# Kernel optimization log

Measured on AMD Instinct MI355X. Metric: run time of the kernel, lower is better.

The kernel has to match this reference:

```python
import jax, jax.numpy as jnp
import numpy as np

H, C = 4, 32          # heads, per-head channels (hidden_dim = 128)
HID = H * C
NC, NM, E, DIN = 100000, 20000, 400000, 64


def _gat_conv(x_src, x_dst, src, dst, Wsrc, Wdst, asrc, adst, bias):
    """PyG-style bipartite GATConv: gather -> leaky-relu attention -> segment softmax -> scatter."""
    n_dst = x_dst.shape[0]
    hs = (x_src @ Wsrc).reshape(-1, H, C)            # [Ns, H, C]
    hd = (x_dst @ Wdst).reshape(-1, H, C)            # [Nd, H, C]
    a_s = jnp.sum(hs * asrc, axis=-1)                # [Ns, H]
    a_d = jnp.sum(hd * adst, axis=-1)                # [Nd, H]
    e = jax.nn.leaky_relu(a_s[src] + a_d[dst], 0.2)  # [E, H]
    m = jax.ops.segment_max(e, dst, num_segments=n_dst)
    m = jnp.where(jnp.isfinite(m), m, 0.0)           # isolated dst nodes -> -inf max
    ex = jnp.exp(e - m[dst])
    den = jax.ops.segment_sum(ex, dst, num_segments=n_dst)
    alpha = ex / (den[dst] + 1e-16)                  # per-destination segment softmax
    out = jax.ops.segment_sum(hs[src] * alpha[:, :, None], dst, num_segments=n_dst)
    return out.reshape(n_dst, HID) + bias            # concat heads + bias


def _mlp2(x, W1, b1, W2, b2):
    return jax.nn.relu(x @ W1 + b1) @ W2 + b2


def setup_inputs():
    key = jax.random.key(0)
    ks = iter(jax.random.split(key, 80))
    def rn(shape, s):
        return jax.random.normal(next(ks), shape, dtype=jnp.float32) * s
    inp = {}
    inp['x_card'] = rn((NC, DIN), 1.0)
    inp['x_merchant'] = rn((NM, DIN), 1.0)
    for l, din in ((0, DIN), (1, HID)):
        for et in ('cm', 'mc'):
            p = 'l%d_%s_' % (l, et)
            g = (2.0 / (din + HID)) ** 0.5
            inp[p + 'Wsrc'] = rn((din, HID), g)
            inp[p + 'Wdst'] = rn((din, HID), g)
            inp[p + 'asrc'] = rn((H, C), 0.1)
            inp[p + 'adst'] = rn((H, C), 0.1)
            inp[p + 'b'] = jnp.zeros((HID,), jnp.float32)
    for nt in ('card', 'merchant'):
        inp['attw_' + nt] = rn((HID, 1), 0.05)
        inp['attb_' + nt] = jnp.zeros((1,), jnp.float32)
    for nt in ('card', 'mer'):
        inp['cls_%s_W1' % nt] = rn((HID, HID // 2), 0.05)
        inp['cls_%s_b1' % nt] = jnp.zeros((HID // 2,), jnp.float32)
        inp['cls_%s_W2' % nt] = rn((HID // 2, 2), 0.05)
        inp['cls_%s_b2' % nt] = jnp.zeros((2,), jnp.float32)
    inp['risk_W1'] = rn((HID, HID // 2), 0.05)
    inp['risk_b1'] = jnp.zeros((HID // 2,), jnp.float32)
    inp['risk_W2'] = rn((HID // 2, 1), 0.05)
    inp['risk_b2'] = jnp.zeros((1,), jnp.float32)
    inp['cm_src'] = jax.random.randint(next(ks), (E,), 0, NC, dtype=jnp.int32)
    inp['cm_dst'] = jax.random.randint(next(ks), (E,), 0, NM, dtype=jnp.int32)
    inp['mc_src'] = jax.random.randint(next(ks), (E,), 0, NM, dtype=jnp.int32)
    inp['mc_dst'] = jax.random.randint(next(ks), (E,), 0, NC, dtype=jnp.int32)
    return inp


def reference(x_card, x_merchant,
              l0_cm_Wsrc, l0_cm_Wdst, l0_cm_asrc, l0_cm_adst, l0_cm_b,
              l0_mc_Wsrc, l0_mc_Wdst, l0_mc_asrc, l0_mc_adst, l0_mc_b,
              l1_cm_Wsrc, l1_cm_Wdst, l1_cm_asrc, l1_cm_adst, l1_cm_b,
              l1_mc_Wsrc, l1_mc_Wdst, l1_mc_asrc, l1_mc_adst, l1_mc_b,
              attw_card, attb_card, attw_merchant, attb_merchant,
              cls_card_W1, cls_card_b1, cls_card_W2, cls_card_b2,
              cls_mer_W1, cls_mer_b1, cls_mer_W2, cls_mer_b2,
              risk_W1, risk_b1, risk_W2, risk_b2,
              cm_src, cm_dst, mc_src, mc_dst):
    xc, xm = x_card, x_merchant
    # HeteroConv layer 0 (each dst type receives exactly one edge type, so mean-aggr is identity)
    xm1 = _gat_conv(xc, xm, cm_src, cm_dst, l0_cm_Wsrc, l0_cm_Wdst, l0_cm_asrc, l0_cm_adst, l0_cm_b)
    xc1 = _gat_conv(xm, xc, mc_src, mc_dst, l0_mc_Wsrc, l0_mc_Wdst, l0_mc_asrc, l0_mc_adst, l0_mc_b)
    # HeteroConv layer 1
    xm2 = _gat_conv(xc1, xm1, cm_src, cm_dst, l1_cm_Wsrc, l1_cm_Wdst, l1_cm_asrc, l1_cm_adst, l1_cm_b)
    xc2 = _gat_conv(xm1, xc1, mc_src, mc_dst, l1_mc_Wsrc, l1_mc_Wdst, l1_mc_asrc, l1_mc_adst, l1_mc_b)
    # graph-level attention: softmax over the node dimension (dim=0), then reweight
    xc2 = xc2 * jax.nn.softmax(xc2 @ attw_card + attb_card, axis=0)
    xm2 = xm2 * jax.nn.softmax(xm2 @ attw_merchant + attb_merchant, axis=0)
    pred_c = _mlp2(xc2, cls_card_W1, cls_card_b1, cls_card_W2, cls_card_b2)
    pred_m = _mlp2(xm2, cls_mer_W1, cls_mer_b1, cls_mer_W2, cls_mer_b2)
    risk_c = jax.nn.sigmoid(_mlp2(xc2, risk_W1, risk_b1, risk_W2, risk_b2))[:, 0]
    risk_m = jax.nn.sigmoid(_mlp2(xm2, risk_W1, risk_b1, risk_W2, risk_b2))[:, 0]
    return (xc2, xm2, pred_c, pred_m, risk_c, risk_m)
```

## Files before the change

### kernel.cpp

```cpp
#include <hip/hip_runtime.h>

typedef _Float16 f16;
typedef _Float16 f16x2 __attribute__((ext_vector_type(2)));
typedef _Float16 f16x4 __attribute__((ext_vector_type(4)));
typedef _Float16 f16x8 __attribute__((ext_vector_type(8)));
typedef float floatx4 __attribute__((ext_vector_type(4)));

constexpr int NC = 100000;
constexpr int NM = 20000;
constexpr int NE = 400000;

constexpr int OFF_XM2 = NC * 128;
constexpr int OFF_PC  = OFF_XM2 + NM * 128;
constexpr int OFF_PM  = OFF_PC + NC * 2;
constexpr int OFF_RC  = OFF_PM + NM * 2;
constexpr int OFF_RM  = OFF_RC + NC;

__device__ __forceinline__ int bpermi(int v, int srclane) {
  return __builtin_amdgcn_ds_bpermute(srclane << 2, v);
}
__device__ __forceinline__ float bpermf(float v, int srclane) {
  int r = __builtin_amdgcn_ds_bpermute(srclane << 2, __builtin_bit_cast(int, v));
  return __builtin_bit_cast(float, r);
}

__global__ void __launch_bounds__(256) k_prep(
    int* zero_base, int nzero, int* stats_i,
    const float* W0, const float* a0, float* v0,
    const float* W1, const float* a1, float* v1,
    const float* W2, const float* a2, float* v2,
    const float* W3, const float* a3, float* v3,
    const float* cb1, const float* mb1, const float* rb1, float* bC, float* bM,
    const float* S0, const float* S1, const float* S2, const float* S3,
    const float* c1, const float* m1, const float* r1,
    f16* BfL0cm, f16* BfL0mc, f16* BfL1cm, f16* BfL1mc, f16* BfC, f16* BfM) {
  int b = blockIdx.x, t = threadIdx.x;
  if (b < 256) {
    for (int i = b * 256 + t; i < nzero + 4; i += 256 * 256) {
      if (i < nzero) zero_base[i] = 0; else stats_i[i - nzero] = 0;
    }
  } else if (b == 256) {
    const float* Wd[4] = {W0, W1, W2, W3};
    const float* ad[4] = {a0, a1, a2, a3};
    float* vd[4] = {v0, v1, v2, v3};
    for (int idx = t; idx < 1536; idx += 256) {
      int mat, base;
      if (idx < 256)       { mat = 0; base = 0; }
      else if (idx < 512)  { mat = 1; base = 256; }
      else if (idx < 1024) { mat = 2; base = 512; }
      else                 { mat = 3; base = 1024; }
      int local = idx - base, k = local >> 2, h = local & 3;
      const float* W = Wd[mat]; const float* a = ad[mat];
      float s = 0.f;
      for (int c = 0; c < 32; ++c) s += W[k * 128 + h * 32 + c] * a[h * 32 + c];
      vd[mat][local] = s;
    }
    if (t < 128) {
      bC[t] = (t < 64) ? cb1[t] : rb1[t - 64];
      bM[t] = (t < 64) ? mb1[t] : rb1[t - 64];
    }
  } else {
    int s = b - 257;
    const float* Wp = nullptr; const float* cA = nullptr; const float* cB = nullptr;
    f16* dst; int kt;
    if (s < 2)       { Wp = S0; dst = BfL0cm; kt = s; }
    else if (s < 4)  { Wp = S1; dst = BfL0mc; kt = s - 2; }
    else if (s < 8)  { Wp = S2; dst = BfL1cm; kt = s - 4; }
    else if (s < 12) { Wp = S3; dst = BfL1mc; kt = s - 8; }
    else if (s < 16) { cA = c1; cB = r1; dst = BfC; kt = s - 12; }
    else             { cA = m1; cB = r1; dst = BfM; kt = s - 16; }
    for (int e = t; e < 512; e += 256) {
      int lane = e & 63, ct = e >> 6;
      int m = lane & 15, q = lane >> 4;
      int col = ct * 16 + m;
      f16x8 frag;
      #pragma unroll
      for (int j = 0; j < 8; ++j) {
        int k = kt * 32 + q * 8 + j;
        float val = Wp ? Wp[k * 128 + col]
                       : (col < 64 ? cA[k * 64 + col] : cB[k * 64 + (col - 64)]);
        frag[j] = (f16)val;
      }
      *reinterpret_cast<f16x8*>(&dst[(size_t)((kt * 8 + ct) * 64 + lane) * 8]) = frag;
    }
  }
}

__global__ void k_hist(const int* cm_dst, const int* mc_dst, int* cnt_cm, int* cnt_mc) {
  int i = blockIdx.x * blockDim.x + threadIdx.x;
  int stride = gridDim.x * blockDim.x;
  for (; i < NE; i += stride) {
    atomicAdd(&cnt_cm[cm_dst[i]], 1);
    atomicAdd(&cnt_mc[mc_dst[i]], 1);
  }
}

__global__ void __launch_bounds__(256) k_scan1(const int* cnt_cm, const int* cnt_mc,
                                               int* offs_cm, int* offs_mc, int* parts) {
  int b = blockIdx.x;
  const int* cnt; int* offs; int n, chunk;
  if (b < 20) { cnt = cnt_cm; offs = offs_cm; n = NM; chunk = b; }
  else        { cnt = cnt_mc; offs = offs_mc; n = NC; chunk = b - 20; }
  int t = threadIdx.x;
  int base = chunk * 1024;
  int v[4]; int tsum = 0;
  #pragma unroll
  for (int j = 0; j < 4; ++j) {
    int idx = base + t * 4 + j;
    v[j] = (idx < n) ? cnt[idx] : 0;
    tsum += v[j];
  }
  __shared__ int sd[256];
  sd[t] = tsum; __syncthreads();
  for (int off = 1; off < 256; off <<= 1) {
    int x = (t >= off) ? sd[t - off] : 0;
    __syncthreads();
    sd[t] += x;
    __syncthreads();
  }
  int excl = sd[t] - tsum;
  int r = excl;
  #pragma unroll
  for (int j = 0; j < 4; ++j) {
    int idx = base + t * 4 + j;
    if (idx < n) offs[idx] = r;
    r += v[j];
  }
  if (t == 0) parts[b] = sd[255];
}

__global__ void __launch_bounds__(256) k_scan2(int* parts) {
  int b = blockIdx.x;
  int base = (b == 0) ? 0 : 20;
  int n = (b == 0) ? 20 : 98;
  int t = threadIdx.x;
  __shared__ int sd[128];
  int v = 0;
  if (t < 128) { v = (t < n) ? parts[base + t] : 0; sd[t] = v; }
  __syncthreads();
  for (int off = 1; off < 128; off <<= 1) {
    int x = 0;
    if (t < 128 && t >= off) x = sd[t - off];
    __syncthreads();
    if (t < 128) sd[t] += x;
    __syncthreads();
  }
  if (t < 128 && t < n) parts[base + t] = sd[t] - v;
}

__global__ void k_scan3(int* offs_cm, int* offs_mc, int* cur_cm, int* cur_mc, const int* parts) {
  int i = blockIdx.x * blockDim.x + threadIdx.x;
  if (i < NM) {
    int val = offs_cm[i] + parts[i >> 10];
    offs_cm[i] = val; cur_cm[i] = val;
  } else if (i < NM + NC) {
    int j = i - NM;
    int val = offs_mc[j] + parts[20 + (j >> 10)];
    offs_mc[j] = val; cur_mc[j] = val;
  }
  if (i == 0) { offs_cm[NM] = NE; offs_mc[NC] = NE; }
}

__global__ void k_scatter(const int* cm_src, const int* cm_dst,
                          const int* mc_src, const int* mc_dst,
                          int* cur_cm, int* cur_mc, int* csr_cm, int* csr_mc) {
  int i = blockIdx.x * blockDim.x + threadIdx.x;
  int stride = gridDim.x * blockDim.x;
  for (; i < NE; i += stride) {
    int p = atomicAdd(&cur_cm[cm_dst[i]], 1);
    csr_cm[p] = cm_src[i];
    int q = atomicAdd(&cur_mc[mc_dst[i]], 1);
    csr_mc[q] = mc_src[i];
  }
}

struct GemmSide {
  const float* x; const f16* Bf;
  const float* asrc; const float* v; f16* hs; float* asO; float* adO;
  const float* bias; const float* wnum; const float* den; float* outx;
  const float* W2; const float* B2; const float* w2r; const float* b2r;
  float* pred; float* risk;
  int M;
};

template<int K, int EPI>
__global__ void __launch_bounds__(256) k_gemm(GemmSide A, GemmSide B, int gridA) {
  constexpr int PP = K + 8;
  constexpr int F4 = K / 4;
  __shared__ f16 xs16[64 * PP];
  const bool isA = (int)blockIdx.x < gridA;
  GemmSide S = isA ? A : B;
  const int blk = isA ? (int)blockIdx.x : (int)blockIdx.x - gridA;
  const int rows0 = blk * 64;
  const int t = (int)threadIdx.x;
  float invden_s = 0.f;
  if constexpr (EPI == 1) invden_s = 1.0f / S.den[0];
  const float4* x4 = reinterpret_cast<const float4*>(S.x);
  #pragma unroll
  for (int ii = 0; ii < (64 * F4) / 256; ++ii) {
    int idx = t + ii * 256;
    int r = idx / F4, f = idx % F4;
    int gr = rows0 + r;
    float4 val = {0.f, 0.f, 0.f, 0.f};
    if (gr < S.M) val = x4[(size_t)gr * F4 + f];
    f16x4 hv; hv.x = (f16)val.x; hv.y = (f16)val.y; hv.z = (f16)val.z; hv.w = (f16)val.w;
    *reinterpret_cast<f16x4*>(&xs16[r * PP + f * 4]) = hv;
    if constexpr (EPI == 1) {
      if (gr < S.M) {
        float w = S.wnum[gr] * invden_s;
        float4 ov = {val.x * w, val.y * w, val.z * w, val.w * w};
        *reinterpret_cast<float4*>(&S.outx[(size_t)gr * 128 + f * 4]) = ov;
      }
    }
  }
  __syncthreads();
  const int lane = t & 63, w = t >> 6;
  const int m = lane & 15, q = lane >> 4;
  const int rbase = w * 16;
  floatx4 acc[8];
  #pragma unroll
  for (int ct = 0; ct < 8; ++ct) acc[ct] = {0.f, 0.f, 0.f, 0.f};
  const f16x8* Bf8 = reinterpret_cast<const f16x8*>(S.Bf);
  #pragma unroll
  for (int kt = 0; kt < K / 32; ++kt) {
    f16x8 a = *reinterpret_cast<const f16x8*>(&xs16[(rbase + m) * PP + kt * 32 + q * 8]);
    #pragma unroll
    for (int ct = 0; ct < 8; ++ct) {
      f16x8 b = Bf8[(kt * 8 + ct) * 64 + lane];
      acc[ct] = __builtin_amdgcn_mfma_f32_16x16x32_f16(a, b, acc[ct], 0, 0, 0);
    }
  }
  if constexpr (EPI == 0) {
    #pragma unroll
    for (int reg = 0; reg < 4; ++reg) {
      int gr = rows0 + rbase + q * 4 + reg;
      bool ok = gr < S.M;
      #pragma unroll
      for (int cp = 0; cp < 4; ++cp) {
        float v0 = acc[2 * cp][reg], v1 = acc[2 * cp + 1][reg];
        float w0 = __shfl_xor(v0, 1), w1 = __shfl_xor(v1, 1);
        bool even = (m & 1) == 0;
        f16x2 pr;
        pr.x = (f16)(even ? v0 : w1);
        pr.y = (f16)(even ? w0 : v1);
        int col = even ? (2 * cp) * 16 + m : (2 * cp + 1) * 16 + m - 1;
        if (ok) *reinterpret_cast<f16x2*>(&S.hs[(size_t)gr * 128 + col]) = pr;
      }
    }
    float as0[4], as1[4];
    #pragma unroll
    for (int h = 0; h < 4; ++h) { as0[h] = S.asrc[h * 32 + m]; as1[h] = S.asrc[h * 32 + 16 + m]; }
    #pragma unroll
    for (int reg = 0; reg < 4; ++reg) {
      float p[4];
      #pragma unroll
      for (int h = 0; h < 4; ++h)
        p[h] = acc[2 * h][reg] * as0[h] + acc[2 * h + 1][reg] * as1[h];
      #pragma unroll
      for (int off = 1; off < 16; off <<= 1) {
        #pragma unroll
        for (int h = 0; h < 4; ++h) p[h] += __shfl_xor(p[h], off);
      }
      int gr = rows0 + rbase + q * 4 + reg;
      if (m == 0 && gr < S.M) {
        float4 pv = {p[0], p[1], p[2], p[3]};
        *reinterpret_cast<float4*>(&S.asO[gr * 4]) = pv;
      }
    }
    float qd[4] = {0.f, 0.f, 0.f, 0.f};
    const float4* v4p = reinterpret_cast<const float4*>(S.v);
    constexpr int KS = K / 4;
    #pragma unroll
    for (int i = 0; i < KS; ++i) {
      int k = q * KS + i;
      float xv = (float)xs16[(rbase + m) * PP + k];
      float4 vk = v4p[k];
      qd[0] += xv * vk.x; qd[1] += xv * vk.y; qd[2] += xv * vk.z; qd[3] += xv * vk.w;
    }
    #pragma unroll
    for (int h = 0; h < 4; ++h) {
      qd[h] += __shfl_xor(qd[h], 16);
      qd[h] += __shfl_xor(qd[h], 32);
    }
    int gr2 = rows0 + rbase + m;
    if (q == 0 && gr2 < S.M) {
      float4 qv = {qd[0], qd[1], qd[2], qd[3]};
      *reinterpret_cast<float4*>(&S.adO[gr2 * 4]) = qv;
    }
  } else {
    float wn[4];
    #pragma unroll
    for (int reg = 0; reg < 4; ++reg) {
      int gr = rows0 + rbase + q * 4 + reg;
      wn[reg] = (gr < S.M) ? S.wnum[gr] * invden_s : 0.f;
    }
    float bct[8], w2c0[4], w2c1[4], w2rv[4];
    #pragma unroll
    for (int ct = 0; ct < 8; ++ct) bct[ct] = S.bias[ct * 16 + m];
    #pragma unroll
    for (int ct = 0; ct < 4; ++ct) {
      int col = ct * 16 + m;
      w2c0[ct] = S.W2[col * 2];
      w2c1[ct] = S.W2[col * 2 + 1];
      w2rv[ct] = S.w2r[col];
    }
    #pragma unroll
    for (int reg = 0; reg < 4; ++reg) {
      float p0 = 0.f, p1 = 0.f, rr = 0.f;
      #pragma unroll
      for (int ct = 0; ct < 4; ++ct) {
        float hv = fmaxf(acc[ct][reg] * wn[reg] + bct[ct], 0.f);
        p0 += hv * w2c0[ct];
        p1 += hv * w2c1[ct];
      }
      #pragma unroll
      for (int ct = 4; ct < 8; ++ct) {
        float hv = fmaxf(acc[ct][reg] * wn[reg] + bct[ct], 0.f);
        rr += hv * w2rv[ct - 4];
      }
      #pragma unroll
      for (int off = 1; off < 16; off <<= 1) {
        p0 += __shfl_xor(p0, off);
        p1 += __shfl_xor(p1, off);
        rr += __shfl_xor(rr, off);
      }
      int gr = rows0 + rbase + q * 4 + reg;
      if (m == 0 && gr < S.M) {
        float2 pp = {p0 + S.B2[0], p1 + S.B2[1]};
        *reinterpret_cast<float2*>(&S.pred[gr * 2]) = pp;
        float z = rr + S.b2r[0];
        S.risk[gr] = 1.f / (1.f + __expf(-z));
      }
    }
  }
}

struct AggSide {
  const int* offs; const int* csr; const float* as_; const float* ad;
  const f16* hs; const float* bias; float* out;
  const float* attw; const float* attb; float* logv;
};

__global__ void __launch_bounds__(256) k_agg(AggSide A, AggSide B, int ndstA, int ntot) {
  const int wid = (int)blockIdx.x * 4 + ((int)threadIdx.x >> 6);
  if (wid >= ntot) return;
  const bool isA = wid < ndstA;
  const AggSide S = isA ? A : B;
  const int d = isA ? wid : wid - ndstA;
  const int lane = (int)threadIdx.x & 63;
  const int we = lane >> 2, wh = lane & 3;
  const int ep = lane >> 5;
  const int c4 = lane & 31;
  const int gh = c4 >> 3;
  const int c8 = c4 << 3;
  const int wh4 = wh << 2;
  const int beg = __builtin_amdgcn_readfirstlane(S.offs[d]);
  const int end = __builtin_amdgcn_readfirstlane(S.offs[d + 1]);
  const float adv = S.ad[d * 4 + wh];
  const char* __restrict__ hsb = (const char*)S.hs;
  const char* __restrict__ asb = (const char*)S.as_;
  float m_run = -1e30f, den = 0.f;
  float acc0 = 0.f, acc1 = 0.f, acc2 = 0.f, acc3 = 0.f;
  for (int base = beg; base < end; base += 16) {
    const int n = min(16, end - base);
    int sb = 0; float e = -1e30f;
    if (we < n) {
      int s = S.csr[base + we];
      sb = s << 8;
      float asv = *reinterpret_cast<const float*>(asb + (unsigned)((s << 4) + wh4));
      float ev = asv + adv;
      e = (ev > 0.f) ? ev : 0.2f * ev;
    }
    float cm = e;
    cm = fmaxf(cm, __shfl_xor(cm, 4));
    cm = fmaxf(cm, __shfl_xor(cm, 8));
    if (n > 4) cm = fmaxf(cm, __shfl_xor(cm, 16));
    if (n > 8) cm = fmaxf(cm, __shfl_xor(cm, 32));
    const float m_new = fmaxf(m_run, cm);
    const float scale = __expf(m_run - m_new);
    const float w = __expf(e - m_new);
    float ws = w;
    ws += __shfl_xor(ws, 4);
    ws += __shfl_xor(ws, 8);
    if (n > 4) ws += __shfl_xor(ws, 16);
    if (n > 8) ws += __shfl_xor(ws, 32);
    den = den * scale + ws;
    m_run = m_new;
    const float sg = bpermf(scale, gh);
    acc0 *= sg; acc1 *= sg; acc2 *= sg; acc3 *= sg;
    int j = 0;
    for (; j + 8 <= n; j += 8) {
      int i0 = (j + ep) << 2, i1 = (j + 2 + ep) << 2;
      int i2 = (j + 4 + ep) << 2, i3 = (j + 6 + ep) << 2;
      int s0 = bpermi(sb, i0);
      int s1 = bpermi(sb, i1);
      int s2 = bpermi(sb, i2);
      int s3 = bpermi(sb, i3);
      f16x4 h0 = *reinterpret_cast<const f16x4*>(hsb + (unsigned)(s0 + c8));
      f16x4 h1 = *reinterpret_cast<const f16x4*>(hsb + (unsigned)(s1 + c8));
      f16x4 h2 = *reinterpret_cast<const f16x4*>(hsb + (unsigned)(s2 + c8));
      f16x4 h3 = *reinterpret_cast<const f16x4*>(hsb + (unsigned)(s3 + c8));
      float w0 = bpermf(w, i0 + gh);
      float w1 = bpermf(w, i1 + gh);
      float w2 = bpermf(w, i2 + gh);
      float w3 = bpermf(w, i3 + gh);
      acc0 += w0 * (float)h0.x; acc1 += w0 * (float)h0.y;
      acc2 += w0 * (float)h0.z; acc3 += w0 * (float)h0.w;
      acc0 += w1 * (float)h1.x; acc1 += w1 * (float)h1.y;
      acc2 += w1 * (float)h1.z; acc3 += w1 * (float)h1.w;
      acc0 += w2 * (float)h2.x; acc1 += w2 * (float)h2.y;
      acc2 += w2 * (float)h2.z; acc3 += w2 * (float)h2.w;
      acc0 += w3 * (float)h3.x; acc1 += w3 * (float)h3.y;
      acc2 += w3 * (float)h3.z; acc3 += w3 * (float)h3.w;
    }
    for (; j + 4 <= n; j += 4) {
      int i0 = (j + ep) << 2, i1 = (j + 2 + ep) << 2;
      int s0 = bpermi(sb, i0);
      int s1 = bpermi(sb, i1);
      f16x4 h0 = *reinterpret_cast<const f16x4*>(hsb + (unsigned)(s0 + c8));
      f16x4 h1 = *reinterpret_cast<const f16x4*>(hsb + (unsigned)(s1 + c8));
      float w0 = bpermf(w, i0 + gh);
      float w1 = bpermf(w, i1 + gh);
      acc0 += w0 * (float)h0.x; acc1 += w0 * (float)h0.y;
      acc2 += w0 * (float)h0.z; acc3 += w0 * (float)h0.w;
      acc0 += w1 * (float)h1.x; acc1 += w1 * (float)h1.y;
      acc2 += w1 * (float)h1.z; acc3 += w1 * (float)h1.w;
    }
    for (; j < n; j += 2) {
      int i0 = (j + ep) << 2;
      int s0 = bpermi(sb, i0);
      f16x4 h0 = *reinterpret_cast<const f16x4*>(hsb + (unsigned)(s0 + c8));
      float w0 = bpermf(w, i0 + gh);
      acc0 += w0 * (float)h0.x; acc1 += w0 * (float)h0.y;
      acc2 += w0 * (float)h0.z; acc3 += w0 * (float)h0.w;
    }
  }
  acc0 += __shfl_xor(acc0, 32);
  acc1 += __shfl_xor(acc1, 32);
  acc2 += __shfl_xor(acc2, 32);
  acc3 += __shfl_xor(acc3, 32);
  const float deng = bpermf(den, gh);
  const float invden = (deng > 0.f) ? 1.f / deng : 0.f;
  const float4 b4 = *reinterpret_cast<const float4*>(&S.bias[c4 * 4]);
  float o0 = acc0 * invden + b4.x;
  float o1 = acc1 * invden + b4.y;
  float o2 = acc2 * invden + b4.z;
  float o3 = acc3 * invden + b4.w;
  if (ep == 0) {
    float4 o = {o0, o1, o2, o3};
    *reinterpret_cast<float4*>(&S.out[d * 128 + c4 * 4]) = o;
  }
  if (S.attw) {
    const float4 aw = *reinterpret_cast<const float4*>(&S.attw[c4 * 4]);
    float sl = o0 * aw.x + o1 * aw.y + o2 * aw.z + o3 * aw.w;
    sl += __shfl_xor(sl, 1);
    sl += __shfl_xor(sl, 2);
    sl += __shfl_xor(sl, 4);
    sl += __shfl_xor(sl, 8);
    sl += __shfl_xor(sl, 16);
    if (lane == 0) S.logv[d] = sl + S.attb[0];
  }
}

__global__ void __launch_bounds__(1024) k_stats(const float* logc, const float* logm, float* stats) {
  const float* src = (blockIdx.x == 0) ? logc : logm;
  int n = (blockIdx.x == 0) ? NC : NM;
  float m = -1e30f;
  for (int i = threadIdx.x; i < n; i += 1024) m = fmaxf(m, src[i]);
  __shared__ float sd[1024];
  sd[threadIdx.x] = m; __syncthreads();
  for (int off = 512; off > 0; off >>= 1) {
    if ((int)threadIdx.x < off) sd[threadIdx.x] = fmaxf(sd[threadIdx.x], sd[threadIdx.x + off]);
    __syncthreads();
  }
  if (threadIdx.x == 0) stats[blockIdx.x] = sd[0];
}

__global__ void __launch_bounds__(256) k_expsum(float* logc, float* logm, float* stats) {
  bool card = (int)blockIdx.x < 256;
  float* logv = card ? logc : logm;
  int n = card ? NC : NM;
  float mx = card ? stats[0] : stats[1];
  int b0 = card ? (int)blockIdx.x : (int)blockIdx.x - 256;
  int nb = card ? 256 : 64;
  float local = 0.f;
  for (int i = b0 * 256 + (int)threadIdx.x; i < n; i += nb * 256) {
    float e = __expf(logv[i] - mx);
    logv[i] = e;
    local += e;
  }
  __shared__ float sd[256];
  sd[threadIdx.x] = local; __syncthreads();
  for (int off = 128; off > 0; off >>= 1) {
    if ((int)threadIdx.x < off) sd[threadIdx.x] += sd[threadIdx.x + off];
    __syncthreads();
  }
  if (threadIdx.x == 0) atomicAdd(card ? &stats[2] : &stats[3], sd[0]);
}

extern "C" void kernel_launch(void* const* d_in, const int* in_sizes, int n_in,
                              void* d_out, int out_size, void* d_ws, size_t ws_size,
                              hipStream_t stream) {
  (void)in_sizes; (void)n_in; (void)out_size; (void)ws_size;
  const float* x_card    = (const float*)d_in[0];
  const float* x_mer     = (const float*)d_in[1];
  const float* l0cm_Wsrc = (const float*)d_in[2];
  const float* l0cm_Wdst = (const float*)d_in[3];
  const float* l0cm_asrc = (const float*)d_in[4];
  const float* l0cm_adst = (const float*)d_in[5];
  const float* l0cm_b    = (const float*)d_in[6];
  const float* l0mc_Wsrc = (const float*)d_in[7];
  const float* l0mc_Wdst = (const float*)d_in[8];
  const float* l0mc_asrc = (const float*)d_in[9];
  const float* l0mc_adst = (const float*)d_in[10];
  const float* l0mc_b    = (const float*)d_in[11];
  const float* l1cm_Wsrc = (const float*)d_in[12];
  const float* l1cm_Wdst = (const float*)d_in[13];
  const float* l1cm_asrc = (const float*)d_in[14];
  const float* l1cm_adst = (const float*)d_in[15];
  const float* l1cm_b    = (const float*)d_in[16];
  const float* l1mc_Wsrc = (const float*)d_in[17];
  const float* l1mc_Wdst = (const float*)d_in[18];
  const float* l1mc_asrc = (const float*)d_in[19];
  const float* l1mc_adst = (const float*)d_in[20];
  const float* l1mc_b    = (const float*)d_in[21];
  const float* attw_c    = (const float*)d_in[22];
  const float* attb_c    = (const float*)d_in[23];
  const float* attw_m    = (const float*)d_in[24];
  const float* attb_m    = (const float*)d_in[25];
  const float* clsc_W1   = (const float*)d_in[26];
  const float* clsc_b1   = (const float*)d_in[27];
  const float* clsc_W2   = (const float*)d_in[28];
  const float* clsc_b2   = (const float*)d_in[29];
  const float* clsm_W1   = (const float*)d_in[30];
  const float* clsm_b1   = (const float*)d_in[31];
  const float* clsm_W2   = (const float*)d_in[32];
  const float* clsm_b2   = (const float*)d_in[33];
  const float* risk_W1   = (const float*)d_in[34];
  const float* risk_b1   = (const float*)d_in[35];
  const float* risk_W2   = (const float*)d_in[36];
  const float* risk_b2   = (const float*)d_in[37];
  const int*   cm_src    = (const int*)d_in[38];
  const int*   cm_dst    = (const int*)d_in[39];
  const int*   mc_src    = (const int*)d_in[40];
  const int*   mc_dst    = (const int*)d_in[41];
  float* out = (float*)d_out;

  float* base = (float*)d_ws;
  size_t o = 0;
  auto alloc = [&](size_t n) { float* p = base + o; o += (n + 3) & ~size_t(3); return p; };
  float* hs_card = alloc((size_t)NC * 128);
  float* xc1     = alloc((size_t)NC * 128);
  float* hs_mer  = alloc((size_t)NM * 128);
  float* xm1     = alloc((size_t)NM * 128);
  float* as_card = alloc((size_t)NC * 4);
  float* ad_card = alloc((size_t)NC * 4);
  float* as_mer  = alloc((size_t)NM * 4);
  float* ad_mer  = alloc((size_t)NM * 4);
  float* v_l0cm  = alloc(512);
  float* v_l0mc  = alloc(512);
  float* v_l1cm  = alloc(512);
  float* v_l1mc  = alloc(512);
  float* bC      = alloc(128);
  float* bM      = alloc(128);
  f16* Bf_l0cm = (f16*)alloc(64 * 128 / 2);
  f16* Bf_l0mc = (f16*)alloc(64 * 128 / 2);
  f16* Bf_l1cm = (f16*)alloc(128 * 128 / 2);
  f16* Bf_l1mc = (f16*)alloc(128 * 128 / 2);
  f16* Bf_catC = (f16*)alloc(128 * 128 / 2);
  f16* Bf_catM = (f16*)alloc(128 * 128 / 2);
  float* logc    = alloc(NC);
  float* logm    = alloc(NM);
  float* stats   = alloc(4);
  int* cnt_cm  = (int*)alloc(NM);
  int* cnt_mc  = (int*)alloc(NC);
  int* offs_cm = (int*)alloc(NM + 1);
  int* offs_mc = (int*)alloc(NC + 1);
  int* cur_cm  = (int*)alloc(NM);
  int* cur_mc  = (int*)alloc(NC);
  int* parts   = (int*)alloc(128);
  int* csr_cm  = (int*)alloc(NE);
  int* csr_mc  = (int*)alloc(NE);

  const dim3 B256(256);
  k_prep<<<dim3(277), B256, 0, stream>>>(
      cnt_cm, NM + NC, (int*)stats,
      l0cm_Wdst, l0cm_adst, v_l0cm, l0mc_Wdst, l0mc_adst, v_l0mc,
      l1cm_Wdst, l1cm_adst, v_l1cm, l1mc_Wdst, l1mc_adst, v_l1mc,
      clsc_b1, clsm_b1, risk_b1, bC, bM,
      l0cm_Wsrc, l0mc_Wsrc, l1cm_Wsrc, l1mc_Wsrc,
      clsc_W1, clsm_W1, risk_W1,
      Bf_l0cm, Bf_l0mc, Bf_l1cm, Bf_l1mc, Bf_catC, Bf_catM);
  k_hist<<<dim3(512), B256, 0, stream>>>(cm_dst, mc_dst, cnt_cm, cnt_mc);
  k_scan1<<<dim3(118), B256, 0, stream>>>(cnt_cm, cnt_mc, offs_cm, offs_mc, parts);
  k_scan2<<<dim3(2), B256, 0, stream>>>(parts);
  k_scan3<<<dim3(469), B256, 0, stream>>>(offs_cm, offs_mc, cur_cm, cur_mc, parts);
  k_scatter<<<dim3(512), B256, 0, stream>>>(cm_src, cm_dst, mc_src, mc_dst,
                                            cur_cm, cur_mc, csr_cm, csr_mc);
  const int gA = (NC + 63) / 64;
  const int gB = (NM + 63) / 64;
  const int NTOT = NM + NC;
  const int gAgg = (NTOT + 3) / 4;

  GemmSide sA, sB;
  AggSide aA, aB;
  sA = {x_card, Bf_l0cm, l0cm_asrc, v_l0mc, (f16*)hs_card, as_card, ad_card,
        nullptr, nullptr, nullptr, nullptr, nullptr, nullptr, nullptr, nullptr,
        nullptr, nullptr, NC};
  sB = {x_mer, Bf_l0mc, l0mc_asrc, v_l0cm, (f16*)hs_mer, as_mer, ad_mer,
        nullptr, nullptr, nullptr, nullptr, nullptr, nullptr, nullptr, nullptr,
        nullptr, nullptr, NM};
  k_gemm<64, 0><<<dim3(gA + gB), B256, 0, stream>>>(sA, sB, gA);
  aA = {offs_cm, csr_cm, as_card, ad_mer, (const f16*)hs_card, l0cm_b, xm1,
        nullptr, nullptr, nullptr};
  aB = {offs_mc, csr_mc, as_mer, ad_card, (const f16*)hs_mer, l0mc_b, xc1,
        nullptr, nullptr, nullptr};
  k_agg<<<dim3(gAgg), B256, 0, stream>>>(aA, aB, NM, NTOT);
  sA = {xc1, Bf_l1cm, l1cm_asrc, v_l1mc, (f16*)hs_card, as_card, ad_card,
        nullptr, nullptr, nullptr, nullptr, nullptr, nullptr, nullptr, nullptr,
        nullptr, nullptr, NC};
  sB = {xm1, Bf_l1mc, l1mc_asrc, v_l1cm, (f16*)hs_mer, as_mer, ad_mer,
        nullptr, nullptr, nullptr, nullptr, nullptr, nullptr, nullptr, nullptr,
        nullptr, nullptr, NM};
  k_gemm<128, 0><<<dim3(gA + gB), B256, 0, stream>>>(sA, sB, gA);
  aA = {offs_cm, csr_cm, as_card, ad_mer, (const f16*)hs_card, l1cm_b, xm1,
        attw_m, attb_m, logm};
  aB = {offs_mc, csr_mc, as_mer, ad_card, (const f16*)hs_mer, l1mc_b, xc1,
        attw_c, attb_c, logc};
  k_agg<<<dim3(gAgg), B256, 0, stream>>>(aA, aB, NM, NTOT);
  k_stats<<<dim3(2), dim3(1024), 0, stream>>>(logc, logm, stats);
  k_expsum<<<dim3(320), B256, 0, stream>>>(logc, logm, stats);
  sA = {xc1, Bf_catC, nullptr, nullptr, nullptr, nullptr, nullptr,
        bC, logc, stats + 2, out,
        clsc_W2, clsc_b2, risk_W2, risk_b2,
        out + OFF_PC, out + OFF_RC, NC};
  sB = {xm1, Bf_catM, nullptr, nullptr, nullptr, nullptr, nullptr,
        bM, logm, stats + 3, out + OFF_XM2,
        clsm_W2, clsm_b2, risk_W2, risk_b2,
        out + OFF_PM, out + OFF_RM, NM};
  k_gemm<128, 1><<<dim3(gA + gB), B256, 0, stream>>>(sA, sB, gA);
}
```

Before: 509.7 us.

## Pack two card destinations per wave in GAT aggregation kernel

```diff
diff --git a/kernel.cpp b/kernel.cpp
--- a/kernel.cpp
+++ b/kernel.cpp
@@ -341,124 +341,228 @@
   const float* attw; const float* attb; float* logv;
 };
 
-__global__ void __launch_bounds__(256) k_agg(AggSide A, AggSide B, int ndstA, int ntot) {
+__global__ void __launch_bounds__(256) k_agg(AggSide A, AggSide B,
+                                             int ndstA, int ndstB, int nwaves) {
   const int wid = (int)blockIdx.x * 4 + ((int)threadIdx.x >> 6);
-  if (wid >= ntot) return;
-  const bool isA = wid < ndstA;
-  const AggSide S = isA ? A : B;
-  const int d = isA ? wid : wid - ndstA;
+  if (wid >= nwaves) return;
   const int lane = (int)threadIdx.x & 63;
-  const int we = lane >> 2, wh = lane & 3;
-  const int ep = lane >> 5;
-  const int c4 = lane & 31;
-  const int gh = c4 >> 3;
-  const int c8 = c4 << 3;
-  const int wh4 = wh << 2;
-  const int beg = __builtin_amdgcn_readfirstlane(S.offs[d]);
-  const int end = __builtin_amdgcn_readfirstlane(S.offs[d + 1]);
-  const float adv = S.ad[d * 4 + wh];
-  const char* __restrict__ hsb = (const char*)S.hs;
-  const char* __restrict__ asb = (const char*)S.as_;
-  float m_run = -1e30f, den = 0.f;
-  float acc0 = 0.f, acc1 = 0.f, acc2 = 0.f, acc3 = 0.f;
-  for (int base = beg; base < end; base += 16) {
-    const int n = min(16, end - base);
-    int sb = 0; float e = -1e30f;
-    if (we < n) {
-      int s = S.csr[base + we];
-      sb = s << 8;
-      float asv = *reinterpret_cast<const float*>(asb + (unsigned)((s << 4) + wh4));
-      float ev = asv + adv;
-      e = (ev > 0.f) ? ev : 0.2f * ev;
-    }
-    float cm = e;
-    cm = fmaxf(cm, __shfl_xor(cm, 4));
-    cm = fmaxf(cm, __shfl_xor(cm, 8));
-    if (n > 4) cm = fmaxf(cm, __shfl_xor(cm, 16));
-    if (n > 8) cm = fmaxf(cm, __shfl_xor(cm, 32));
-    const float m_new = fmaxf(m_run, cm);
-    const float scale = __expf(m_run - m_new);
-    const float w = __expf(e - m_new);
-    float ws = w;
-    ws += __shfl_xor(ws, 4);
-    ws += __shfl_xor(ws, 8);
-    if (n > 4) ws += __shfl_xor(ws, 16);
-    if (n > 8) ws += __shfl_xor(ws, 32);
-    den = den * scale + ws;
-    m_run = m_new;
-    const float sg = bpermf(scale, gh);
-    acc0 *= sg; acc1 *= sg; acc2 *= sg; acc3 *= sg;
-    int j = 0;
-    for (; j + 8 <= n; j += 8) {
-      int i0 = (j + ep) << 2, i1 = (j + 2 + ep) << 2;
-      int i2 = (j + 4 + ep) << 2, i3 = (j + 6 + ep) << 2;
-      int s0 = bpermi(sb, i0);
-      int s1 = bpermi(sb, i1);
-      int s2 = bpermi(sb, i2);
-      int s3 = bpermi(sb, i3);
-      f16x4 h0 = *reinterpret_cast<const f16x4*>(hsb + (unsigned)(s0 + c8));
-      f16x4 h1 = *reinterpret_cast<const f16x4*>(hsb + (unsigned)(s1 + c8));
-      f16x4 h2 = *reinterpret_cast<const f16x4*>(hsb + (unsigned)(s2 + c8));
-      f16x4 h3 = *reinterpret_cast<const f16x4*>(hsb + (unsigned)(s3 + c8));
-      float w0 = bpermf(w, i0 + gh);
-      float w1 = bpermf(w, i1 + gh);
-      float w2 = bpermf(w, i2 + gh);
-      float w3 = bpermf(w, i3 + gh);
-      acc0 += w0 * (float)h0.x; acc1 += w0 * (float)h0.y;
-      acc2 += w0 * (float)h0.z; acc3 += w0 * (float)h0.w;
-      acc0 += w1 * (float)h1.x; acc1 += w1 * (float)h1.y;
-      acc2 += w1 * (float)h1.z; acc3 += w1 * (float)h1.w;
-      acc0 += w2 * (float)h2.x; acc1 += w2 * (float)h2.y;
-      acc2 += w2 * (float)h2.z; acc3 += w2 * (float)h2.w;
-      acc0 += w3 * (float)h3.x; acc1 += w3 * (float)h3.y;
-      acc2 += w3 * (float)h3.z; acc3 += w3 * (float)h3.w;
-    }
-    for (; j + 4 <= n; j += 4) {
-      int i0 = (j + ep) << 2, i1 = (j + 2 + ep) << 2;
-      int s0 = bpermi(sb, i0);
-      int s1 = bpermi(sb, i1);
-      f16x4 h0 = *reinterpret_cast<const f16x4*>(hsb + (unsigned)(s0 + c8));
-      f16x4 h1 = *reinterpret_cast<const f16x4*>(hsb + (unsigned)(s1 + c8));
-      float w0 = bpermf(w, i0 + gh);
-      float w1 = bpermf(w, i1 + gh);
-      acc0 += w0 * (float)h0.x; acc1 += w0 * (float)h0.y;
-      acc2 += w0 * (float)h0.z; acc3 += w0 * (float)h0.w;
-      acc0 += w1 * (float)h1.x; acc1 += w1 * (float)h1.y;
-      acc2 += w1 * (float)h1.z; acc3 += w1 * (float)h1.w;
-    }
-    for (; j < n; j += 2) {
-      int i0 = (j + ep) << 2;
-      int s0 = bpermi(sb, i0);
-      f16x4 h0 = *reinterpret_cast<const f16x4*>(hsb + (unsigned)(s0 + c8));
-      float w0 = bpermf(w, i0 + gh);
-      acc0 += w0 * (float)h0.x; acc1 += w0 * (float)h0.y;
-      acc2 += w0 * (float)h0.z; acc3 += w0 * (float)h0.w;
-    }
-  }
-  acc0 += __shfl_xor(acc0, 32);
-  acc1 += __shfl_xor(acc1, 32);
-  acc2 += __shfl_xor(acc2, 32);
-  acc3 += __shfl_xor(acc3, 32);
-  const float deng = bpermf(den, gh);
-  const float invden = (deng > 0.f) ? 1.f / deng : 0.f;
-  const float4 b4 = *reinterpret_cast<const float4*>(&S.bias[c4 * 4]);
-  float o0 = acc0 * invden + b4.x;
-  float o1 = acc1 * invden + b4.y;
-  float o2 = acc2 * invden + b4.z;
-  float o3 = acc3 * invden + b4.w;
-  if (ep == 0) {
-    float4 o = {o0, o1, o2, o3};
-    *reinterpret_cast<float4*>(&S.out[d * 128 + c4 * 4]) = o;
-  }
-  if (S.attw) {
-    const float4 aw = *reinterpret_cast<const float4*>(&S.attw[c4 * 4]);
-    float sl = o0 * aw.x + o1 * aw.y + o2 * aw.z + o3 * aw.w;
-    sl += __shfl_xor(sl, 1);
-    sl += __shfl_xor(sl, 2);
-    sl += __shfl_xor(sl, 4);
-    sl += __shfl_xor(sl, 8);
-    sl += __shfl_xor(sl, 16);
-    if (lane == 0) S.logv[d] = sl + S.attb[0];
+  if (wid < ndstA) {
+    const AggSide S = A;
+    const int d = wid;
+    const int we = lane >> 2, wh = lane & 3;
+    const int ep = lane >> 5;
+    const int c4 = lane & 31;
+    const int gh = c4 >> 3;
+    const int c8 = c4 << 3;
+    const int wh4 = wh << 2;
+    const int beg = __builtin_amdgcn_readfirstlane(S.offs[d]);
+    const int end = __builtin_amdgcn_readfirstlane(S.offs[d + 1]);
+    const float adv = S.ad[d * 4 + wh];
+    const char* __restrict__ hsb = (const char*)S.hs;
+    const char* __restrict__ asb = (const char*)S.as_;
+    float m_run = -1e30f, den = 0.f;
+    float acc0 = 0.f, acc1 = 0.f, acc2 = 0.f, acc3 = 0.f;
+    for (int base = beg; base < end; base += 16) {
+      const int n = min(16, end - base);
+      int sb = 0; float e = -1e30f;
+      if (we < n) {
+        int s = S.csr[base + we];
+        sb = s << 8;
+        float asv = *reinterpret_cast<const float*>(asb + (unsigned)((s << 4) + wh4));
+        float ev = asv + adv;
+        e = (ev > 0.f) ? ev : 0.2f * ev;
+      }
+      float cm = e;
+      cm = fmaxf(cm, __shfl_xor(cm, 4));
+      cm = fmaxf(cm, __shfl_xor(cm, 8));
+      if (n > 4) cm = fmaxf(cm, __shfl_xor(cm, 16));
+      if (n > 8) cm = fmaxf(cm, __shfl_xor(cm, 32));
+      const float m_new = fmaxf(m_run, cm);
+      const float scale = __expf(m_run - m_new);
+      const float w = __expf(e - m_new);
+      float ws = w;
+      ws += __shfl_xor(ws, 4);
+      ws += __shfl_xor(ws, 8);
+      if (n > 4) ws += __shfl_xor(ws, 16);
+      if (n > 8) ws += __shfl_xor(ws, 32);
+      den = den * scale + ws;
+      m_run = m_new;
+      const float sg = bpermf(scale, gh);
+      acc0 *= sg; acc1 *= sg; acc2 *= sg; acc3 *= sg;
+      int j = 0;
+      for (; j + 8 <= n; j += 8) {
+        int i0 = (j + ep) << 2, i1 = (j + 2 + ep) << 2;
+        int i2 = (j + 4 + ep) << 2, i3 = (j + 6 + ep) << 2;
+        int s0 = bpermi(sb, i0);
+        int s1 = bpermi(sb, i1);
+        int s2 = bpermi(sb, i2);
+        int s3 = bpermi(sb, i3);
+        f16x4 h0 = *reinterpret_cast<const f16x4*>(hsb + (unsigned)(s0 + c8));
+        f16x4 h1 = *reinterpret_cast<const f16x4*>(hsb + (unsigned)(s1 + c8));
+        f16x4 h2 = *reinterpret_cast<const f16x4*>(hsb + (unsigned)(s2 + c8));
+        f16x4 h3 = *reinterpret_cast<const f16x4*>(hsb + (unsigned)(s3 + c8));
+        float w0 = bpermf(w, i0 + gh);
+        float w1 = bpermf(w, i1 + gh);
+        float w2 = bpermf(w, i2 + gh);
+        float w3 = bpermf(w, i3 + gh);
+        acc0 += w0 * (float)h0.x; acc1 += w0 * (float)h0.y;
+        acc2 += w0 * (float)h0.z; acc3 += w0 * (float)h0.w;
+        acc0 += w1 * (float)h1.x; acc1 += w1 * (float)h1.y;
+        acc2 += w1 * (float)h1.z; acc3 += w1 * (float)h1.w;
+        acc0 += w2 * (float)h2.x; acc1 += w2 * (float)h2.y;
+        acc2 += w2 * (float)h2.z; acc3 += w2 * (float)h2.w;
+        acc0 += w3 * (float)h3.x; acc1 += w3 * (float)h3.y;
+        acc2 += w3 * (float)h3.z; acc3 += w3 * (float)h3.w;
+      }
+      for (; j + 4 <= n; j += 4) {
+        int i0 = (j + ep) << 2, i1 = (j + 2 + ep) << 2;
+        int s0 = bpermi(sb, i0);
+        int s1 = bpermi(sb, i1);
+        f16x4 h0 = *reinterpret_cast<const f16x4*>(hsb + (unsigned)(s0 + c8));
+        f16x4 h1 = *reinterpret_cast<const f16x4*>(hsb + (unsigned)(s1 + c8));
+        float w0 = bpermf(w, i0 + gh);
+        float w1 = bpermf(w, i1 + gh);
+        acc0 += w0 * (float)h0.x; acc1 += w0 * (float)h0.y;
+        acc2 += w0 * (float)h0.z; acc3 += w0 * (float)h0.w;
+        acc0 += w1 * (float)h1.x; acc1 += w1 * (float)h1.y;
+        acc2 += w1 * (float)h1.z; acc3 += w1 * (float)h1.w;
+      }
+      for (; j < n; j += 2) {
+        int i0 = (j + ep) << 2;
+        int s0 = bpermi(sb, i0);
+        f16x4 h0 = *reinterpret_cast<const f16x4*>(hsb + (unsigned)(s0 + c8));
+        float w0 = bpermf(w, i0 + gh);
+        acc0 += w0 * (float)h0.x; acc1 += w0 * (float)h0.y;
+        acc2 += w0 * (float)h0.z; acc3 += w0 * (float)h0.w;
+      }
+    }
+    acc0 += __shfl_xor(acc0, 32);
+    acc1 += __shfl_xor(acc1, 32);
+    acc2 += __shfl_xor(acc2, 32);
+    acc3 += __shfl_xor(acc3, 32);
+    const float deng = bpermf(den, gh);
+    const float invden = (deng > 0.f) ? 1.f / deng : 0.f;
+    const float4 b4 = *reinterpret_cast<const float4*>(&S.bias[c4 * 4]);
+    float o0 = acc0 * invden + b4.x;
+    float o1 = acc1 * invden + b4.y;
+    float o2 = acc2 * invden + b4.z;
+    float o3 = acc3 * invden + b4.w;
+    if (ep == 0) {
+      float4 o = {o0, o1, o2, o3};
+      *reinterpret_cast<float4*>(&S.out[d * 128 + c4 * 4]) = o;
+    }
+    if (S.attw) {
+      const float4 aw = *reinterpret_cast<const float4*>(&S.attw[c4 * 4]);
+      float sl = o0 * aw.x + o1 * aw.y + o2 * aw.z + o3 * aw.w;
+      sl += __shfl_xor(sl, 1);
+      sl += __shfl_xor(sl, 2);
+      sl += __shfl_xor(sl, 4);
+      sl += __shfl_xor(sl, 8);
+      sl += __shfl_xor(sl, 16);
+      if (lane == 0) S.logv[d] = sl + S.attb[0];
+    }
+  } else {
+    const AggSide S = B;
+    const int p = wid - ndstA;
+    const int half32 = lane & 32;
+    const int l5 = lane & 31;
+    int d = p * 2 + (lane >> 5);
+    const bool dok = d < ndstB;
+    if (!dok) d = ndstB - 1;
+    const int we = l5 >> 2, wh = l5 & 3;
+    const int gh = l5 >> 3;
+    const int c8 = l5 << 3;
+    const char* __restrict__ hsb = (const char*)S.hs;
+    const char* __restrict__ asb = (const char*)S.as_;
+    const int beg = S.offs[d];
+    const int end = dok ? S.offs[d + 1] : beg;
+    const float adv = S.ad[d * 4 + wh];
+    int nch = (end - beg + 7) >> 3;
+    int nco = __shfl_xor(nch, 32);
+    const int ncmax = __builtin_amdgcn_readfirstlane(max(nch, nco));
+    float m_run = -1e30f, den = 0.f;
+    float acc0 = 0.f, acc1 = 0.f, acc2 = 0.f, acc3 = 0.f;
+    for (int cc = 0; cc < ncmax; ++cc) {
+      const int n = min(end - beg - cc * 8, 8);
+      int sb = 0; float e = -1e30f;
+      const bool wv = we < n;
+      if (wv) {
+        int s = S.csr[beg + cc * 8 + we];
+        sb = s << 8;
+        float asv = *reinterpret_cast<const float*>(asb + (unsigned)((s << 4) + (wh << 2)));
+        float ev = asv + adv;
+        e = (ev > 0.f) ? ev : 0.2f * ev;
+      }
+      float cm = e;
+      cm = fmaxf(cm, __shfl_xor(cm, 4));
+      cm = fmaxf(cm, __shfl_xor(cm, 8));
+      cm = fmaxf(cm, __shfl_xor(cm, 16));
+      const float m_new = fmaxf(m_run, cm);
+      const float scale = __expf(m_run - m_new);
+      const float w = wv ? __expf(e - m_new) : 0.f;
+      float ws = w;
+      ws += __shfl_xor(ws, 4);
+      ws += __shfl_xor(ws, 8);
+      ws += __shfl_xor(ws, 16);
+      den = den * scale + ws;
+      m_run = m_new;
+      acc0 *= scale; acc1 *= scale; acc2 *= scale; acc3 *= scale;
+      int jv = max(n, 0);
+      int jo = __shfl_xor(jv, 32);
+      const int jm = __builtin_amdgcn_readfirstlane(max(jv, jo));
+      int j = 0;
+      for (; j + 4 <= jm; j += 4) {
+        int i0 = half32 + j * 4, i1 = i0 + 4, i2 = i0 + 8, i3 = i0 + 12;
+        int s0 = bpermi(sb, i0);
+        int s1 = bpermi(sb, i1);
+        int s2 = bpermi(sb, i2);
+        int s3 = bpermi(sb, i3);
+        f16x4 h0 = *reinterpret_cast<const f16x4*>(hsb + (unsigned)(s0 + c8));
+        f16x4 h1 = *reinterpret_cast<const f16x4*>(hsb + (unsigned)(s1 + c8));
+        f16x4 h2 = *reinterpret_cast<const f16x4*>(hsb + (unsigned)(s2 + c8));
+        f16x4 h3 = *reinterpret_cast<const f16x4*>(hsb + (unsigned)(s3 + c8));
+        float w0 = bpermf(w, i0 + gh);
+        float w1 = bpermf(w, i1 + gh);
+        float w2 = bpermf(w, i2 + gh);
+        float w3 = bpermf(w, i3 + gh);
+        acc0 += w0 * (float)h0.x; acc1 += w0 * (float)h0.y;
+        acc2 += w0 * (float)h0.z; acc3 += w0 * (float)h0.w;
+        acc0 += w1 * (float)h1.x; acc1 += w1 * (float)h1.y;
+        acc2 += w1 * (float)h1.z; acc3 += w1 * (float)h1.w;
+        acc0 += w2 * (float)h2.x; acc1 += w2 * (float)h2.y;
+        acc2 += w2 * (float)h2.z; acc3 += w2 * (float)h2.w;
+        acc0 += w3 * (float)h3.x; acc1 += w3 * (float)h3.y;
+        acc2 += w3 * (float)h3.z; acc3 += w3 * (float)h3.w;
+      }
+      for (; j < jm; ++j) {
+        int i0 = half32 + j * 4;
+        int s0 = bpermi(sb, i0);
+        f16x4 h0 = *reinterpret_cast<const f16x4*>(hsb + (unsigned)(s0 + c8));
+        float w0 = bpermf(w, i0 + gh);
+        acc0 += w0 * (float)h0.x; acc1 += w0 * (float)h0.y;
+        acc2 += w0 * (float)h0.z; acc3 += w0 * (float)h0.w;
+      }
+    }
+    const float invden = (den > 0.f) ? 1.f / den : 0.f;
+    const float4 b4 = *reinterpret_cast<const float4*>(&S.bias[l5 * 4]);
+    float o0 = acc0 * invden + b4.x;
+    float o1 = acc1 * invden + b4.y;
+    float o2 = acc2 * invden + b4.z;
+    float o3 = acc3 * invden + b4.w;
+    if (dok) {
+      float4 o = {o0, o1, o2, o3};
+      *reinterpret_cast<float4*>(&S.out[d * 128 + l5 * 4]) = o;
+    }
+    if (S.attw) {
+      const float4 aw = *reinterpret_cast<const float4*>(&S.attw[l5 * 4]);
+      float sl = o0 * aw.x + o1 * aw.y + o2 * aw.z + o3 * aw.w;
+      sl += __shfl_xor(sl, 1);
+      sl += __shfl_xor(sl, 2);
+      sl += __shfl_xor(sl, 4);
+      sl += __shfl_xor(sl, 8);
+      sl += __shfl_xor(sl, 16);
+      if (l5 == 0 && dok) S.logv[d] = sl + S.attb[0];
+    }
   }
 }
 
@@ -599,8 +703,8 @@
                                             cur_cm, cur_mc, csr_cm, csr_mc);
   const int gA = (NC + 63) / 64;
   const int gB = (NM + 63) / 64;
-  const int NTOT = NM + NC;
-  const int gAgg = (NTOT + 3) / 4;
+  const int NWAVES = NM + (NC + 1) / 2;
+  const int gAgg = (NWAVES + 3) / 4;
 
   GemmSide sA, sB;
   AggSide aA, aB;
@@ -615,7 +719,7 @@
         nullptr, nullptr, nullptr};
   aB = {offs_mc, csr_mc, as_mer, ad_card, (const f16*)hs_mer, l0mc_b, xc1,
         nullptr, nullptr, nullptr};
-  k_agg<<<dim3(gAgg), B256, 0, stream>>>(aA, aB, NM, NTOT);
+  k_agg<<<dim3(gAgg), B256, 0, stream>>>(aA, aB, NM, NC, NWAVES);
   sA = {xc1, Bf_l1cm, l1cm_asrc, v_l1mc, (f16*)hs_card, as_card, ad_card,
         nullptr, nullptr, nullptr, nullptr, nullptr, nullptr, nullptr, nullptr,
         nullptr, nullptr, NC};
@@ -627,7 +731,7 @@
         attw_m, attb_m, logm};
   aB = {offs_mc, csr_mc, as_mer, ad_card, (const f16*)hs_mer, l1mc_b, xc1,
         attw_c, attb_c, logc};
-  k_agg<<<dim3(gAgg), B256, 0, stream>>>(aA, aB, NM, NTOT);
+  k_agg<<<dim3(gAgg), B256, 0, stream>>>(aA, aB, NM, NC, NWAVES);
   k_stats<<<dim3(2), dim3(1024), 0, stream>>>(logc, logm, stats);
   k_expsum<<<dim3(320), B256, 0, stream>>>(logc, logm, stats);
   sA = {xc1, Bf_catC, nullptr, nullptr, nullptr, nullptr, nullptr,
```

Measured after the change: 486.3 us. -4.6%, faster.
